# Kernel optimization log

Hardware: AMD Instinct MI355X
Metric: run time of the kernel (lower is better)

The kernel has to match this reference:

```python
import jax, jax.numpy as jnp
import numpy as np

DIM = 3                     # bits consumed per tree level
FBITS = 1 << DIM            # 8 occupancy bits per flag
K = 4                       # set bits per flag (enforced in setup_inputs -> static level sizes)
BITS_PER_DIM = [10, 10, 10]
WORD_LENGTH = sum(BITS_PER_DIM)          # 30
TREE_DEPTH = int(np.ceil(WORD_LENGTH / DIM))  # 10
PERMUTE = np.arange(WORD_LENGTH)[::-1].copy() # bit-reversal permutation
TOTAL_FLAGS = sum(K ** t for t in range(TREE_DEPTH))  # 349525
N_POINTS = K ** TREE_DEPTH                            # 1048576


def _make_flags(total, seed=0):
    # each flag has exactly K of FBITS bits set -> deterministic level sizes
    rng = np.random.default_rng(seed)
    r = rng.random((total, FBITS))
    idx = np.argsort(r, axis=1)[:, :K]          # K distinct bit positions
    flags = np.bitwise_or.reduce(1 << idx, axis=1).astype(np.int32)
    return flags


def setup_inputs() -> dict:
    key = jax.random.key(0)
    k1, k2 = jax.random.split(key)
    flags = jnp.asarray(_make_flags(TOTAL_FLAGS))
    offset = jax.random.normal(k1, (3,), dtype=jnp.float32)
    scale = jax.random.uniform(k2, (3,), dtype=jnp.float32) + 0.5
    return {"flags": flags, "offset": offset, "scale": scale}


def reference(flags, offset, scale):
    bit_range = jnp.arange(FBITS, dtype=jnp.int32)
    X = jnp.zeros((1,), dtype=jnp.int32)
    pos = 0
    # bitops.decode loop: each set bit j of flag i spawns child (X[i] << DIM) | j
    for t in range(TREE_DEPTH):
        n = K ** t  # nodes at this level (static by input construction)
        seg = jax.lax.dynamic_slice(flags, (pos,), (n,))
        bits = (seg[:, None] >> bit_range) & 1            # [n, FBITS]
        i, x = jnp.nonzero(bits == 1, size=n * K)         # row-major, matches tf.where
        X = x.astype(jnp.int32) + (X << DIM)[i]           # [n*K]
        pos += n
    # bitops.permute: scatter each bit b of X to position PERMUTE[b]
    b = (X[:, None] >> jnp.arange(WORD_LENGTH, dtype=jnp.int32)) & 1   # [N, 30]
    X = jnp.sum(b << jnp.asarray(PERMUTE, dtype=jnp.int32), axis=-1)  # [N]
    # bitops.realize: split word into per-dim fields, cast, scale, offset
    masks = jnp.asarray([(1 << bb) - 1 for bb in BITS_PER_DIM], dtype=jnp.int32)
    shifts = jnp.asarray(np.cumsum([0] + BITS_PER_DIM[:-1]), dtype=jnp.int32)
    Xf = ((X[:, None] >> shifts) & masks).astype(jnp.float32)          # [N, 3]
    return Xf * scale + offset
```

## Files before the change

### kernel.cpp

```cpp
#include <hip/hip_runtime.h>


__device__ __forceinline__ unsigned sel_bit(unsigned f, unsigned d) {
    if (d > 0u) f &= f - 1u;
    if (d > 1u) f &= f - 1u;
    if (d > 2u) f &= f - 1u;
    return (unsigned)__builtin_ctz(f);
}

__device__ __forceinline__ unsigned swz(unsigned s) {
    return s ^ ((s >> 3) & 7u);
}

__global__ __launch_bounds__(256) void nbit_tree_decode(
    const int* __restrict__ flags,
    const float* __restrict__ off3,
    const float* __restrict__ scl3,
    float* __restrict__ out)
{
    constexpr unsigned LOFF[10] = {0u, 1u, 5u, 21u, 85u, 341u, 1365u, 5461u, 21845u, 87381u};

    const unsigned tid = threadIdx.x;
    const unsigned q = blockIdx.x * 256u + tid;

    const unsigned qw = __builtin_amdgcn_readfirstlane(q);
    unsigned Xs = 0u;
#pragma unroll
    for (int t = 0; t < 6; ++t) {
        const unsigned i = qw >> (18 - 2 * t);
        const unsigned d = (qw >> (16 - 2 * t)) & 3u;
        const unsigned f = (unsigned)flags[LOFF[t] + i];
        Xs = (Xs << 3) | sel_bit(f, d);
    }

    unsigned Xv = 0u;
#pragma unroll
    for (int t = 6; t < 9; ++t) {
        const unsigned i = q >> (18 - 2 * t);
        const unsigned d = (q >> (16 - 2 * t)) & 3u;
        const unsigned f = (unsigned)flags[LOFF[t] + i];
        Xv = (Xv << 3) | sel_bit(f, d);
    }
    const unsigned base = ((Xs << 9) | Xv) << 3;

    const unsigned f9 = (unsigned)flags[LOFF[9] + q];

    const float s0 = scl3[0], s1 = scl3[1], s2 = scl3[2];
    const float o0 = off3[0], o1 = off3[1], o2 = off3[2];

    float4 v[3];
    float* vf = (float*)v;
    unsigned f = f9;
#pragma unroll
    for (int d = 0; d < 4; ++d) {
        const unsigned j = (unsigned)__builtin_ctz(f);
        f &= f - 1u;
        const unsigned X  = base | j;
        const unsigned Xr = __brev(X) >> 2;
        vf[3 * d + 0] = fmaf((float)(Xr & 1023u),         s0, o0);
        vf[3 * d + 1] = fmaf((float)((Xr >> 10) & 1023u), s1, o1);
        vf[3 * d + 2] = fmaf((float)((Xr >> 20) & 1023u), s2, o2);
    }

    __shared__ float4 stage[768];
#pragma unroll
    for (int k = 0; k < 3; ++k)
        stage[swz(3u * tid + k)] = v[k];
    __syncthreads();

    float4* og = (float4*)out + (size_t)blockIdx.x * 768u;
#pragma unroll
    for (int k = 0; k < 3; ++k) {
        const unsigned s = 256u * k + tid;
        og[s] = stage[swz(s)];
    }
}

extern "C" void kernel_launch(void* const* d_in, const int* in_sizes, int n_in,
                              void* d_out, int out_size, void* d_ws, size_t ws_size,
                              hipStream_t stream) {
    const int*   flags  = (const int*)d_in[0];
    const float* offset = (const float*)d_in[1];
    const float* scale  = (const float*)d_in[2];
    float*       out    = (float*)d_out;

    nbit_tree_decode<<<dim3(1024), dim3(256), 0, stream>>>(flags, offset, scale, out);
}
```

Before: 62.80 us.

## Assign one output point per thread and launch four times more blocks

Each thread now decodes a single leaf point instead of all four children of a level-9 flag, so the grid grows from 1024 to 4096 blocks. Levels 0-6 are resolved wave-uniformly through readfirstlane, and each thread then does levels 7, 8 and 9 itself, with lane bits picking the child. The aim is more parallelism and fewer registers per thread, and the output is staged through unswizzled shared memory with 192 threads doing the float4 stores. In exchange the upper-level flag loads and bit selections are repeated about four times overall, and a quarter of the threads sit idle during the store phase.

```diff
diff --git a/kernel.cpp b/kernel.cpp
--- a/kernel.cpp
+++ b/kernel.cpp
@@ -6,10 +6,6 @@
     if (d > 1u) f &= f - 1u;
     if (d > 2u) f &= f - 1u;
     return (unsigned)__builtin_ctz(f);
-}
-
-__device__ __forceinline__ unsigned swz(unsigned s) {
-    return s ^ ((s >> 3) & 7u);
 }
 
 __global__ __launch_bounds__(256) void nbit_tree_decode(
@@ -21,58 +17,43 @@
     constexpr unsigned LOFF[10] = {0u, 1u, 5u, 21u, 85u, 341u, 1365u, 5461u, 21845u, 87381u};
 
     const unsigned tid = threadIdx.x;
-    const unsigned q = blockIdx.x * 256u + tid;
+    const unsigned g   = blockIdx.x * 256u + tid;
+    const unsigned q   = g >> 2;
+    const unsigned dl  = g & 3u;
 
     const unsigned qw = __builtin_amdgcn_readfirstlane(q);
     unsigned Xs = 0u;
 #pragma unroll
-    for (int t = 0; t < 6; ++t) {
+    for (int t = 0; t < 7; ++t) {
         const unsigned i = qw >> (18 - 2 * t);
         const unsigned d = (qw >> (16 - 2 * t)) & 3u;
         const unsigned f = (unsigned)flags[LOFF[t] + i];
         Xs = (Xs << 3) | sel_bit(f, d);
     }
 
-    unsigned Xv = 0u;
-#pragma unroll
-    for (int t = 6; t < 9; ++t) {
-        const unsigned i = q >> (18 - 2 * t);
-        const unsigned d = (q >> (16 - 2 * t)) & 3u;
-        const unsigned f = (unsigned)flags[LOFF[t] + i];
-        Xv = (Xv << 3) | sel_bit(f, d);
-    }
-    const unsigned base = ((Xs << 9) | Xv) << 3;
+    const unsigned f7 = (unsigned)flags[LOFF[7] + (qw >> 4)];
+    unsigned X = (Xs << 3) | sel_bit(f7, (q >> 2) & 3u);
+
+    const unsigned f8 = (unsigned)flags[LOFF[8] + (q >> 2)];
+    X = (X << 3) | sel_bit(f8, q & 3u);
 
     const unsigned f9 = (unsigned)flags[LOFF[9] + q];
+    X = (X << 3) | sel_bit(f9, dl);
+
+    const unsigned Xr = __brev(X) >> 2;
 
     const float s0 = scl3[0], s1 = scl3[1], s2 = scl3[2];
     const float o0 = off3[0], o1 = off3[1], o2 = off3[2];
 
-    float4 v[3];
-    float* vf = (float*)v;
-    unsigned f = f9;
-#pragma unroll
-    for (int d = 0; d < 4; ++d) {
-        const unsigned j = (unsigned)__builtin_ctz(f);
-        f &= f - 1u;
-        const unsigned X  = base | j;
-        const unsigned Xr = __brev(X) >> 2;
-        vf[3 * d + 0] = fmaf((float)(Xr & 1023u),         s0, o0);
-        vf[3 * d + 1] = fmaf((float)((Xr >> 10) & 1023u), s1, o1);
-        vf[3 * d + 2] = fmaf((float)((Xr >> 20) & 1023u), s2, o2);
-    }
-
-    __shared__ float4 stage[768];
-#pragma unroll
-    for (int k = 0; k < 3; ++k)
-        stage[swz(3u * tid + k)] = v[k];
+    __shared__ __align__(16) float stage[768];
+    stage[3u * tid + 0u] = fmaf((float)(Xr & 1023u),         s0, o0);
+    stage[3u * tid + 1u] = fmaf((float)((Xr >> 10) & 1023u), s1, o1);
+    stage[3u * tid + 2u] = fmaf((float)((Xr >> 20) & 1023u), s2, o2);
     __syncthreads();
 
-    float4* og = (float4*)out + (size_t)blockIdx.x * 768u;
-#pragma unroll
-    for (int k = 0; k < 3; ++k) {
-        const unsigned s = 256u * k + tid;
-        og[s] = stage[swz(s)];
+    if (tid < 192u) {
+        float4* og = (float4*)out + (size_t)blockIdx.x * 192u;
+        og[tid] = ((const float4*)stage)[tid];
     }
 }
 
@@ -84,5 +65,5 @@
     const float* scale  = (const float*)d_in[2];
     float*       out    = (float*)d_out;
 
-    nbit_tree_decode<<<dim3(1024), dim3(256), 0, stream>>>(flags, offset, scale, out);
+    nbit_tree_decode<<<dim3(4096), dim3(256), 0, stream>>>(flags, offset, scale, out);
 }
```

Result: slower. 66.87 us (+6.5%).

## Decode two level-8 children per thread and factor the shared bit-reversed prefix

Applied to the files above, without the earlier changes.

Each thread now handles two last-level flags (eight points) that share a level-8 parent, so the path walk for levels 0-8 is done once per pair and the grid is halved. The reversed prefix is computed once and the x/y coordinates are reused across the four leaves. Only the z coordinate varies, and it is built from the leaf bits with a byte permute and one FMA. Shared-memory staging doubles to 1536 float4 per block, which raises per-block LDS use and halves the number of blocks available for latency hiding.

```diff
diff --git a/kernel.cpp b/kernel.cpp
--- a/kernel.cpp
+++ b/kernel.cpp
@@ -21,56 +21,68 @@
     constexpr unsigned LOFF[10] = {0u, 1u, 5u, 21u, 85u, 341u, 1365u, 5461u, 21845u, 87381u};
 
     const unsigned tid = threadIdx.x;
-    const unsigned q = blockIdx.x * 256u + tid;
+    const unsigned u   = blockIdx.x * 256u + tid;
 
-    const unsigned qw = __builtin_amdgcn_readfirstlane(q);
-    unsigned Xs = 0u;
+    const unsigned uw = __builtin_amdgcn_readfirstlane(u);
+    unsigned P = 0u;
 #pragma unroll
-    for (int t = 0; t < 6; ++t) {
-        const unsigned i = qw >> (18 - 2 * t);
-        const unsigned d = (qw >> (16 - 2 * t)) & 3u;
+    for (int t = 0; t < 5; ++t) {
+        const unsigned i = uw >> (17 - 2 * t);
+        const unsigned d = (uw >> (15 - 2 * t)) & 3u;
         const unsigned f = (unsigned)flags[LOFF[t] + i];
-        Xs = (Xs << 3) | sel_bit(f, d);
+        P = (P << 3) | sel_bit(f, d);
     }
+    {
+        const unsigned f5 = (unsigned)flags[LOFF[5] + (uw >> 7)];
+        P = (P << 3) | sel_bit(f5, (u >> 5) & 3u);
+    }
+    {
+        const unsigned f6 = (unsigned)flags[LOFF[6] + (u >> 5)];
+        P = (P << 3) | sel_bit(f6, (u >> 3) & 3u);
+        const unsigned f7 = (unsigned)flags[LOFF[7] + (u >> 3)];
+        P = (P << 3) | sel_bit(f7, (u >> 1) & 3u);
+    }
+    const unsigned f8   = (unsigned)flags[LOFF[8] + (u >> 1)];
+    const unsigned e    = (u & 1u) << 1;
+    const unsigned b8_0 = sel_bit(f8, e);
+    const unsigned b8_1 = sel_bit(f8, e | 1u);
 
-    unsigned Xv = 0u;
-#pragma unroll
-    for (int t = 6; t < 9; ++t) {
-        const unsigned i = q >> (18 - 2 * t);
-        const unsigned d = (q >> (16 - 2 * t)) & 3u;
-        const unsigned f = (unsigned)flags[LOFF[t] + i];
-        Xv = (Xv << 3) | sel_bit(f, d);
-    }
-    const unsigned base = ((Xs << 9) | Xv) << 3;
-
-    const unsigned f9 = (unsigned)flags[LOFF[9] + q];
+    const unsigned f9_0 = (unsigned)flags[LOFF[9] + (u << 1)];
+    const unsigned f9_1 = (unsigned)flags[LOFF[9] + (u << 1) + 1u];
 
     const float s0 = scl3[0], s1 = scl3[1], s2 = scl3[2];
     const float o0 = off3[0], o1 = off3[1], o2 = off3[2];
+    const float s2x128 = s2 * 128.0f;
 
-    float4 v[3];
-    float* vf = (float*)v;
-    unsigned f = f9;
+    __shared__ __align__(16) float4 stage[1536];
+
 #pragma unroll
-    for (int d = 0; d < 4; ++d) {
-        const unsigned j = (unsigned)__builtin_ctz(f);
-        f &= f - 1u;
-        const unsigned X  = base | j;
-        const unsigned Xr = __brev(X) >> 2;
-        vf[3 * d + 0] = fmaf((float)(Xr & 1023u),         s0, o0);
-        vf[3 * d + 1] = fmaf((float)((Xr >> 10) & 1023u), s1, o1);
-        vf[3 * d + 2] = fmaf((float)((Xr >> 20) & 1023u), s2, o2);
+    for (int n = 0; n < 2; ++n) {
+        const unsigned b8     = n ? b8_1 : b8_0;
+        unsigned       f9     = n ? f9_1 : f9_0;
+        const unsigned base27 = (P << 3) | b8;
+        const unsigned Rb = __brev(base27) >> 5;
+        const float v0  = fmaf((float)(Rb & 1023u),         s0, o0);
+        const float v1  = fmaf((float)((Rb >> 10) & 1023u), s1, o1);
+        const float v2b = fmaf((float)(Rb >> 20),           s2, o2);
+        float w[4];
+#pragma unroll
+        for (int d = 0; d < 4; ++d) {
+            const unsigned j = (unsigned)__builtin_ctz(f9);
+            f9 &= f9 - 1u;
+            const unsigned ji = __builtin_amdgcn_perm(0x07030501u, 0x06020400u, j);
+            w[d] = fmaf((float)ji, s2x128, v2b);
+        }
+        const unsigned sb = 6u * tid + 3u * (unsigned)n;
+        stage[swz(sb + 0u)] = make_float4(v0,   v1,   w[0], v0);
+        stage[swz(sb + 1u)] = make_float4(v1,   w[1], v0,   v1);
+        stage[swz(sb + 2u)] = make_float4(w[2], v0,   v1,   w[3]);
     }
-
-    __shared__ float4 stage[768];
-#pragma unroll
-    for (int k = 0; k < 3; ++k)
-        stage[swz(3u * tid + k)] = v[k];
     __syncthreads();
 
-    float4* og = (float4*)out + (size_t)blockIdx.x * 768u;
+    float4* og = (float4*)out + (size_t)blockIdx.x * 1536u;
 #pragma unroll
-    for (int k = 0; k < 3; ++k) {
+    for (int k = 0; k < 6; ++k) {
         const unsigned s = 256u * k + tid;
         og[s] = stage[swz(s)];
     }
@@ -84,5 +96,5 @@
     const float* scale  = (const float*)d_in[2];
     float*       out    = (float*)d_out;
 
-    nbit_tree_decode<<<dim3(1024), dim3(256), 0, stream>>>(flags, offset, scale, out);
+    nbit_tree_decode<<<dim3(512), dim3(256), 0, stream>>>(flags, offset, scale, out);
 }
```

Measured after the change: 63.68 us. Within noise of the previous version (+1.4%).
